# Kernel optimization log

Measured on AMD Instinct MI355X. Metric: run time of the kernel, lower is better.

The kernel has to match this reference:

```python
import jax, jax.numpy as jnp
import numpy as np

NUM_HEADS = 8

def setup_inputs() -> dict:
    key = jax.random.key(0)
    kx, kk, kq, kv, ko = jax.random.split(key, 5)
    B, S, D_in, D_e = 2, 4096, 512, 512
    scale = 1.0 / np.sqrt(D_in)
    x = jax.random.normal(kx, (B, S, D_in), dtype=jnp.float32)
    # nn.Linear(in, out, bias=False) weight has shape (out, in); y = x @ W.T
    W_K = jax.random.normal(kk, (D_e, D_in), dtype=jnp.float32) * scale
    W_Q = jax.random.normal(kq, (D_e, D_in), dtype=jnp.float32) * scale
    W_V = jax.random.normal(kv, (D_e, D_in), dtype=jnp.float32) * scale
    W_O = jax.random.normal(ko, (D_e, D_e), dtype=jnp.float32) * (1.0 / np.sqrt(D_e))
    return {"x": x, "W_K": W_K, "W_Q": W_Q, "W_V": W_V, "W_O": W_O}

def reference(x, W_K, W_Q, W_V, W_O):
    B, S, _ = x.shape
    E = W_K.shape[0]
    H = NUM_HEADS
    d = E // H
    # projections (bias-free linears): y = x @ W.T
    K = jnp.einsum('bsi,ei->bse', x, W_K).reshape(B, S, H, d)
    Q = jnp.einsum('bsi,ei->bse', x, W_Q).reshape(B, S, H, d)
    V = jnp.einsum('bsi,ei->bse', x, W_V).reshape(B, S, H, d)
    # scores with NON-standard scaling: divide by full embed_dim E
    scores = jnp.einsum('bqhd,bkhd->bhqk', Q, K) / E
    weights = jax.nn.softmax(scores, axis=-1)
    wV = jnp.einsum('bhqk,bkhd->bqhd', weights, V).reshape(B, S, E)
    out = jnp.einsum('bse,oe->bso', wV, W_O)
    return out
```

## Files before the change

### kernel.cpp

```cpp
#include <hip/hip_runtime.h>

typedef unsigned short u16;
typedef __attribute__((ext_vector_type(8))) short bf16x8;
typedef __attribute__((ext_vector_type(4))) float f32x4;
typedef __attribute__((ext_vector_type(16))) float f32x16;
typedef __attribute__((ext_vector_type(4))) unsigned int u32x4;

__device__ __forceinline__ u16 f2bf(float f) {
  unsigned u = __builtin_bit_cast(unsigned, f);
  u = u + 0x7fffu + ((u >> 16) & 1u);
  return (u16)(u >> 16);
}

__device__ __forceinline__ float bf2f(u16 u) {
  return __builtin_bit_cast(float, (unsigned)u << 16);
}

__device__ __forceinline__ void gload16(const void* g, void* l) {
  __builtin_amdgcn_global_load_lds((const __attribute__((address_space(1))) unsigned*)g,
                                   (__attribute__((address_space(3))) unsigned*)l, 16, 0, 0);
}

#define MFMA16(a, b, c) __builtin_amdgcn_mfma_f32_16x16x32_bf16(a, b, c, 0, 0, 0)
#define MFMA32(a, b, c) __builtin_amdgcn_mfma_f32_32x32x16_bf16(a, b, c, 0, 0, 0)

__global__ void cvt_kernel(const float* __restrict__ src, u16* __restrict__ dst, int n4, float scale) {
  int i = blockIdx.x * blockDim.x + threadIdx.x;
  if (i >= n4) return;
  const float4 v = ((const float4*)src)[i];
  ushort4 o;
  o.x = f2bf(v.x * scale);
  o.y = f2bf(v.y * scale);
  o.z = f2bf(v.z * scale);
  o.w = f2bf(v.w * scale);
  ((ushort4*)dst)[i] = o;
}

__global__ __launch_bounds__(256) void cvtw_kernel(const float* __restrict__ Wk,
                                                   const float* __restrict__ Wq,
                                                   const float* __restrict__ Wv,
                                                   const float* __restrict__ Wo,
                                                   u16* __restrict__ w1, u16* __restrict__ wo) {
  int i = blockIdx.x * 256 + threadIdx.x;
  int sel = i >> 16, j = i & 65535;
  const float* src = (sel == 0) ? Wk : (sel == 1) ? Wq : (sel == 2) ? Wv : Wo;
  float scale = (sel == 1) ? (1.4426950408889634f / 512.0f) : 1.0f;
  const float4 v = ((const float4*)src)[j];
  ushort4 o;
  o.x = f2bf(v.x * scale);
  o.y = f2bf(v.y * scale);
  o.z = f2bf(v.z * scale);
  o.w = f2bf(v.w * scale);
  if (sel < 3) ((ushort4*)w1)[sel * 65536 + j] = o;
  else         ((ushort4*)wo)[j] = o;
}

template <typename CT>
__global__ __launch_bounds__(256, 2) void gemm_bt(const u16* __restrict__ A,
                                                  const u16* __restrict__ B,
                                                  CT* __restrict__ C, int M, int N, int K,
                                                  u16* __restrict__ VT) {
  __shared__ u16 As[128 * 32];
  __shared__ u16 Bs[128 * 32];
  const int t = threadIdx.x;
  const int lane = t & 63;
  const int w = t >> 6, wr = w >> 1, wc = w & 1;
  const int fr = lane & 15, fq = lane >> 4;
  const long m0 = (long)blockIdx.x * 128, n0 = (long)blockIdx.y * 128;

  f32x4 acc[4][4] = {};

  const int sr = t >> 2;
  const int sc = (t & 3) * 8;
  const u16* Ab = A + (m0 + sr) * (long)K + sc;
  const u16* Bb = B + (n0 + sr) * (long)K + sc;

  for (int k0 = 0; k0 < K; k0 += 32) {
    gload16(Ab + k0, As + t * 8);
    gload16(Ab + 64 * (long)K + k0, As + 2048 + t * 8);
    gload16(Bb + k0, Bs + t * 8);
    gload16(Bb + 64 * (long)K + k0, Bs + 2048 + t * 8);
    __syncthreads();
    bf16x8 a[4], b[4];
#pragma unroll
    for (int i = 0; i < 4; i++)
      a[i] = *(const bf16x8*)(As + (wr * 64 + i * 16 + fr) * 32 + fq * 8);
#pragma unroll
    for (int j = 0; j < 4; j++)
      b[j] = *(const bf16x8*)(Bs + (wc * 64 + j * 16 + fr) * 32 + fq * 8);
#pragma unroll
    for (int i = 0; i < 4; i++)
#pragma unroll
      for (int j = 0; j < 4; j++)
        acc[i][j] = MFMA16(a[i], b[j], acc[i][j]);
    __syncthreads();
  }

  if constexpr (sizeof(CT) == 2) {
    if (VT && n0 >= 1024) {
      const int bb = (int)(m0 >> 12);
      const int s0 = (int)(m0 & 4095) + wr * 64;
      const int hg = (((int)n0 - 1024) >> 6) + wc;
      const long vbase = ((long)(bb * 8 + hg) * 64);
#pragma unroll
      for (int i = 0; i < 4; i++)
#pragma unroll
        for (int j = 0; j < 4; j++) {
          ushort4 o;
          o.x = f2bf(acc[i][j][0]);
          o.y = f2bf(acc[i][j][1]);
          o.z = f2bf(acc[i][j][2]);
          o.w = f2bf(acc[i][j][3]);
          *(ushort4*)(VT + (vbase + j * 16 + fr) * 4096 + s0 + i * 16 + fq * 4) = o;
        }
      return;
    }
  }

#pragma unroll
  for (int i = 0; i < 4; i++)
#pragma unroll
    for (int j = 0; j < 4; j++)
#pragma unroll
      for (int r = 0; r < 4; r++) {
        long m = m0 + wr * 64 + i * 16 + fq * 4 + r;
        long n = n0 + wc * 64 + j * 16 + fr;
        if constexpr (sizeof(CT) == 4)
          C[m * N + n] = acc[i][j][r];
        else
          C[m * N + n] = (CT)f2bf(acc[i][j][r]);
      }
}

template <int NZ>
__global__ __launch_bounds__(512, 4) void attn_kernel(const u16* __restrict__ Y,
                                                      const u16* __restrict__ VT,
                                                      u16* __restrict__ WV,
                                                      u16* __restrict__ PO0,
                                                      u16* __restrict__ PO1,
                                                      float* __restrict__ PD) {
  __shared__ u16 Ks[2][8192];
  __shared__ u16 Vs[2][8192];
  const int t = threadIdx.x;
  const int lane = t & 63, w = t >> 6;
  const int l31 = lane & 31, hi = lane >> 5;
  int orig = blockIdx.x, qb, bh, kh;
  if constexpr (NZ == 2) {
    int logical = (orig & 7) * 64 + (orig >> 3);
    qb = logical & 15; bh = (logical >> 4) & 15; kh = logical >> 8;
  } else {
    int logical = (orig & 7) * 32 + (orig >> 3);
    qb = logical & 15; bh = logical >> 4; kh = 0;
  }
  const int b = bh >> 3, h = bh & 7;
  const long base = (long)b * 4096 * 1536 + h * 64;
  const u16* Kp = Y + base;
  const u16* Qp = Y + base + 512;
  const u16* Vtp = VT + (long)bh * 262144;
  const int q0 = qb * 256 + w * 32;

  int kkv[2], koff[2], vdv[2], voff[2];
#pragma unroll
  for (int r = 0; r < 2; r++) {
    int row = r * 32 + (t >> 4);
    int rx = (t & 15) ^ (row & 15);
    kkv[r] = row * 2 + (rx >> 3);
    koff[r] = (rx & 7) * 8;
    vdv[r] = row;
    voff[r] = rx * 8;
  }

  bf16x8 qf[4];
#pragma unroll
  for (int ks = 0; ks < 4; ks++)
    qf[ks] = *(const bf16x8*)(Qp + (long)(q0 + l31) * 1536 + ks * 16 + hi * 8);

  f32x16 accO[2] = {};
  f32x16 accD = {};
  const u32x4 onesW = {0x3F803F80u, 0x3F803F80u, 0x3F803F80u, 0x3F803F80u};
  const bf16x8 onesB = __builtin_bit_cast(bf16x8, onesW);

  const int kt0 = kh * (32 / NZ), ktN = kt0 + 32 / NZ;

  {
    const int kv0 = kt0 * 128;
#pragma unroll
    for (int r = 0; r < 2; r++) {
      gload16(Kp + (long)(kv0 + kkv[r]) * 1536 + koff[r], &Ks[kt0 & 1][r * 4096 + t * 8]);
      gload16(Vtp + (long)vdv[r] * 4096 + kv0 + voff[r], &Vs[kt0 & 1][r * 4096 + t * 8]);
    }
  }
  __syncthreads();

  for (int kt = kt0; kt < ktN; kt++) {
    const int buf = kt & 1;
    const int kvn = ((kt + 1) & 31) * 128;
#pragma unroll
    for (int r = 0; r < 2; r++) {
      gload16(Kp + (long)(kvn + kkv[r]) * 1536 + koff[r], &Ks[buf ^ 1][r * 4096 + t * 8]);
      gload16(Vtp + (long)vdv[r] * 4096 + kvn + voff[r], &Vs[buf ^ 1][r * 4096 + t * 8]);
    }
    const char* Ksb = (const char*)Ks[buf];
    const char* Vsb = (const char*)Vs[buf];

#pragma unroll
    for (int kv5 = 0; kv5 < 4; kv5++) {
      const int kv = kv5 * 32 + l31;
      const int krow = kv >> 1;
      const int kswz = (krow & 15) << 4;
      const int kpre = ((kv & 1) << 7) | (hi << 4);
      bf16x8 ka[4];
#pragma unroll
      for (int ks = 0; ks < 4; ks++)
        ka[ks] = *(const bf16x8*)(Ksb + krow * 256 + ((kpre | (ks << 5)) ^ kswz));
      f32x16 s0 = {};
#pragma unroll
      for (int ks = 0; ks < 4; ks++)
        s0 = MFMA32(ka[ks], qf[ks], s0);
      unsigned pk0[8];
#pragma unroll
      for (int j = 0; j < 8; j++) {
        float a0 = fmaf(s0[2 * j],     fmaf(s0[2 * j],     0.24022651f, 0.69314718f), 1.0f);
        float a1 = fmaf(s0[2 * j + 1], fmaf(s0[2 * j + 1], 0.24022651f, 0.69314718f), 1.0f);
        pk0[j] = __builtin_amdgcn_perm(__builtin_bit_cast(unsigned, a1),
                                       __builtin_bit_cast(unsigned, a0), 0x07060302u);
      }
#pragma unroll
      for (int s = 0; s < 2; s++) {
        const int bse = s * 4;
        auto rA0 = __builtin_amdgcn_permlane32_swap(pk0[bse + 0], pk0[bse + 2], false, false);
        auto rB0 = __builtin_amdgcn_permlane32_swap(pk0[bse + 1], pk0[bse + 3], false, false);
        u32x4 f0 = {rA0[0], rB0[0], rA0[1], rB0[1]};
        bf16x8 pa0 = __builtin_bit_cast(bf16x8, f0);
        accD = MFMA32(pa0, onesB, accD);
        const int vpre = ((kv5 * 2 + s) << 5) | (hi << 4);
#pragma unroll
        for (int dvb = 0; dvb < 2; dvb++) {
          const int dv = dvb * 32 + l31;
          bf16x8 vb = *(const bf16x8*)(Vsb + dv * 256 + (vpre ^ ((dv & 15) << 4)));
          accO[dvb] = MFMA32(pa0, vb, accO[dvb]);
        }
      }
    }
    __syncthreads();
  }

  const long qgb = (long)b * 4096 + q0;
  if constexpr (NZ == 1) {
#pragma unroll
    for (int r = 0; r < 16; r++) {
      float inv = 1.0f / accD[r];
      long qg = qgb + (r & 3) + 8 * (r >> 2) + 4 * hi;
#pragma unroll
      for (int dvb = 0; dvb < 2; dvb++)
        WV[qg * 512 + h * 64 + dvb * 32 + l31] = f2bf(accO[dvb][r] * inv);
    }
  } else {
    u16* po = kh ? PO1 : PO0;
    float* pd = PD + kh * 65536;
#pragma unroll
    for (int r = 0; r < 16; r++) {
      long qg = qgb + (r & 3) + 8 * (r >> 2) + 4 * hi;
      if (l31 == 0) pd[qg * 8 + h] = accD[r];
#pragma unroll
      for (int dvb = 0; dvb < 2; dvb++)
        po[qg * 512 + h * 64 + dvb * 32 + l31] = f2bf(accO[dvb][r]);
    }
  }
}

__global__ __launch_bounds__(256) void combine_kernel(const u16* __restrict__ PO0,
                                                      const u16* __restrict__ PO1,
                                                      const float* __restrict__ PD,
                                                      u16* __restrict__ WV) {
  int tid = blockIdx.x * 256 + threadIdx.x;
  int q = tid >> 7, e4 = tid & 127;
  int e = e4 * 4, h = e4 >> 4;
  float inv = 1.0f / (PD[q * 8 + h] + PD[65536 + q * 8 + h]);
  ushort4 a = *(const ushort4*)(PO0 + (long)q * 512 + e);
  ushort4 c = *(const ushort4*)(PO1 + (long)q * 512 + e);
  ushort4 o;
  o.x = f2bf((bf2f(a.x) + bf2f(c.x)) * inv);
  o.y = f2bf((bf2f(a.y) + bf2f(c.y)) * inv);
  o.z = f2bf((bf2f(a.z) + bf2f(c.z)) * inv);
  o.w = f2bf((bf2f(a.w) + bf2f(c.w)) * inv);
  *(ushort4*)(WV + (long)q * 512 + e) = o;
}

extern "C" void kernel_launch(void* const* d_in, const int* in_sizes, int n_in,
                              void* d_out, int out_size, void* d_ws, size_t ws_size,
                              hipStream_t stream) {
  (void)in_sizes; (void)n_in; (void)out_size;
  const float* x  = (const float*)d_in[0];
  const float* Wk = (const float*)d_in[1];
  const float* Wq = (const float*)d_in[2];
  const float* Wv = (const float*)d_in[3];
  const float* Wo = (const float*)d_in[4];
  float* out = (float*)d_out;
  char* ws = (char*)d_ws;

  u16* xb = (u16*)ws;
  u16* w1 = (u16*)(ws + 8388608);
  u16* wo = (u16*)(ws + 9961472);
  u16* y  = (u16*)(ws + 10485760);
  u16* wv = (u16*)(ws + 35651584);
  u16* vt = (u16*)(ws + 44040192);
  u16* po1 = (u16*)(ws + 60817408);
  float* pd = (float*)(ws + 69206016);

  cvt_kernel<<<4096, 256, 0, stream>>>(x, xb, 1048576, 1.0f);
  cvtw_kernel<<<1024, 256, 0, stream>>>(Wk, Wq, Wv, Wo, w1, wo);

  gemm_bt<u16><<<dim3(64, 12), 256, 0, stream>>>(xb, w1, y, 8192, 1536, 512, vt);

  if (ws_size >= 69730304ULL) {
    attn_kernel<2><<<512, 512, 0, stream>>>(y, vt, nullptr, xb, po1, pd);
    combine_kernel<<<4096, 256, 0, stream>>>(xb, po1, pd, wv);
  } else {
    attn_kernel<1><<<256, 512, 0, stream>>>(y, vt, wv, nullptr, nullptr, nullptr);
  }
  gemm_bt<float><<<dim3(64, 4), 256, 0, stream>>>(wv, wo, out, 8192, 512, 512, nullptr);
}
```

Before: 124.6 us.

## Fuse split-KV combine into output projection GEMM and merge conversion kernels

Merges the x and weight fp32-to-bf16 conversion kernels into a single launch. It also removes the separate combine kernel: a new output-projection GEMM loads the two partial attention outputs and denominators, normalises them, and writes the bf16 A tile into shared memory before the MFMA loop. This drops two kernel launches and the write-then-read round trip of the combined WV buffer. In exchange, the A operand is loaded synchronously through registers instead of by async global-to-LDS loads, and the GEMM uses smaller 64-row tiles.

Measured after the change: 119.1 us. 4.4% less time.

```diff
diff --git a/kernel.cpp b/kernel.cpp
--- a/kernel.cpp
+++ b/kernel.cpp
@@ -24,35 +24,36 @@
 #define MFMA16(a, b, c) __builtin_amdgcn_mfma_f32_16x16x32_bf16(a, b, c, 0, 0, 0)
 #define MFMA32(a, b, c) __builtin_amdgcn_mfma_f32_32x32x16_bf16(a, b, c, 0, 0, 0)
 
-__global__ void cvt_kernel(const float* __restrict__ src, u16* __restrict__ dst, int n4, float scale) {
-  int i = blockIdx.x * blockDim.x + threadIdx.x;
-  if (i >= n4) return;
-  const float4 v = ((const float4*)src)[i];
-  ushort4 o;
-  o.x = f2bf(v.x * scale);
-  o.y = f2bf(v.y * scale);
-  o.z = f2bf(v.z * scale);
-  o.w = f2bf(v.w * scale);
-  ((ushort4*)dst)[i] = o;
-}
-
-__global__ __launch_bounds__(256) void cvtw_kernel(const float* __restrict__ Wk,
-                                                   const float* __restrict__ Wq,
-                                                   const float* __restrict__ Wv,
-                                                   const float* __restrict__ Wo,
-                                                   u16* __restrict__ w1, u16* __restrict__ wo) {
+__global__ __launch_bounds__(256) void cvt_all(const float* __restrict__ x,
+                                               const float* __restrict__ Wk,
+                                               const float* __restrict__ Wq,
+                                               const float* __restrict__ Wv,
+                                               const float* __restrict__ Wo,
+                                               u16* __restrict__ xb,
+                                               u16* __restrict__ w1,
+                                               u16* __restrict__ wo) {
   int i = blockIdx.x * 256 + threadIdx.x;
-  int sel = i >> 16, j = i & 65535;
-  const float* src = (sel == 0) ? Wk : (sel == 1) ? Wq : (sel == 2) ? Wv : Wo;
-  float scale = (sel == 1) ? (1.4426950408889634f / 512.0f) : 1.0f;
+  const float* src;
+  u16* dst;
+  int j;
+  float scale = 1.0f;
+  if (i < 1048576) {
+    src = x; dst = xb; j = i;
+  } else {
+    int k = i - 1048576;
+    int sel = k >> 16;
+    j = k & 65535;
+    src = (sel == 0) ? Wk : (sel == 1) ? Wq : (sel == 2) ? Wv : Wo;
+    scale = (sel == 1) ? (1.4426950408889634f / 512.0f) : 1.0f;
+    dst = (sel < 3) ? (w1 + (long)sel * 262144) : wo;
+  }
   const float4 v = ((const float4*)src)[j];
   ushort4 o;
   o.x = f2bf(v.x * scale);
   o.y = f2bf(v.y * scale);
   o.z = f2bf(v.z * scale);
   o.w = f2bf(v.w * scale);
-  if (sel < 3) ((ushort4*)w1)[sel * 65536 + j] = o;
-  else         ((ushort4*)wo)[j] = o;
+  ((ushort4*)dst)[j] = o;
 }
 
 template <typename CT>
@@ -129,6 +130,72 @@
           C[m * N + n] = acc[i][j][r];
         else
           C[m * N + n] = (CT)f2bf(acc[i][j][r]);
+      }
+}
+
+__global__ __launch_bounds__(256, 2) void gemm_out(const u16* __restrict__ PO0,
+                                                   const u16* __restrict__ PO1,
+                                                   const float* __restrict__ PD,
+                                                   const u16* __restrict__ B,
+                                                   float* __restrict__ C) {
+  __shared__ u16 As[64 * 32];
+  __shared__ u16 Bs[128 * 32];
+  const int t = threadIdx.x;
+  const int lane = t & 63;
+  const int w = t >> 6, wr = w >> 1, wc = w & 1;
+  const int fr = lane & 15, fq = lane >> 4;
+  const long m0 = (long)blockIdx.x * 64, n0 = (long)blockIdx.y * 128;
+
+  f32x4 acc[2][4] = {};
+
+  const int ar = t >> 2;
+  const int sc = (t & 3) * 8;
+  const long q = m0 + ar;
+  const u16* Ap0 = PO0 + q * 512 + sc;
+  const u16* Ap1 = PO1 + q * 512 + sc;
+  const u16* Bb = B + (n0 + (t >> 2)) * 512L + sc;
+
+  for (int k0 = 0; k0 < 512; k0 += 32) {
+    gload16(Bb + k0, Bs + t * 8);
+    gload16(Bb + 64 * 512 + k0, Bs + 2048 + t * 8);
+    {
+      const int h = (k0 + sc) >> 6;
+      float inv = 1.0f / (PD[q * 8 + h] + PD[65536 + q * 8 + h]);
+      u32x4 o0 = *(const u32x4*)(Ap0 + k0);
+      u32x4 o1 = *(const u32x4*)(Ap1 + k0);
+      u32x4 pk;
+#pragma unroll
+      for (int e = 0; e < 4; e++) {
+        float lo = (bf2f((u16)(o0[e] & 0xffff)) + bf2f((u16)(o1[e] & 0xffff))) * inv;
+        float hi = (bf2f((u16)(o0[e] >> 16)) + bf2f((u16)(o1[e] >> 16))) * inv;
+        pk[e] = (unsigned)f2bf(lo) | ((unsigned)f2bf(hi) << 16);
+      }
+      *(u32x4*)(As + t * 8) = pk;
+    }
+    __syncthreads();
+    bf16x8 a[2], b[4];
+#pragma unroll
+    for (int i = 0; i < 2; i++)
+      a[i] = *(const bf16x8*)(As + (wr * 32 + i * 16 + fr) * 32 + fq * 8);
+#pragma unroll
+    for (int j = 0; j < 4; j++)
+      b[j] = *(const bf16x8*)(Bs + (wc * 64 + j * 16 + fr) * 32 + fq * 8);
+#pragma unroll
+    for (int i = 0; i < 2; i++)
+#pragma unroll
+      for (int j = 0; j < 4; j++)
+        acc[i][j] = MFMA16(a[i], b[j], acc[i][j]);
+    __syncthreads();
+  }
+#pragma unroll
+  for (int i = 0; i < 2; i++)
+#pragma unroll
+    for (int j = 0; j < 4; j++)
+#pragma unroll
+      for (int r = 0; r < 4; r++) {
+        long m = m0 + wr * 32 + i * 16 + fq * 4 + r;
+        long n = n0 + wc * 64 + j * 16 + fr;
+        C[m * 512 + n] = acc[i][j][r];
       }
 }
 
@@ -269,24 +336,6 @@
   }
 }
 
-__global__ __launch_bounds__(256) void combine_kernel(const u16* __restrict__ PO0,
-                                                      const u16* __restrict__ PO1,
-                                                      const float* __restrict__ PD,
-                                                      u16* __restrict__ WV) {
-  int tid = blockIdx.x * 256 + threadIdx.x;
-  int q = tid >> 7, e4 = tid & 127;
-  int e = e4 * 4, h = e4 >> 4;
-  float inv = 1.0f / (PD[q * 8 + h] + PD[65536 + q * 8 + h]);
-  ushort4 a = *(const ushort4*)(PO0 + (long)q * 512 + e);
-  ushort4 c = *(const ushort4*)(PO1 + (long)q * 512 + e);
-  ushort4 o;
-  o.x = f2bf((bf2f(a.x) + bf2f(c.x)) * inv);
-  o.y = f2bf((bf2f(a.y) + bf2f(c.y)) * inv);
-  o.z = f2bf((bf2f(a.z) + bf2f(c.z)) * inv);
-  o.w = f2bf((bf2f(a.w) + bf2f(c.w)) * inv);
-  *(ushort4*)(WV + (long)q * 512 + e) = o;
-}
-
 extern "C" void kernel_launch(void* const* d_in, const int* in_sizes, int n_in,
                               void* d_out, int out_size, void* d_ws, size_t ws_size,
                               hipStream_t stream) {
@@ -308,16 +357,15 @@
   u16* po1 = (u16*)(ws + 60817408);
   float* pd = (float*)(ws + 69206016);
 
-  cvt_kernel<<<4096, 256, 0, stream>>>(x, xb, 1048576, 1.0f);
-  cvtw_kernel<<<1024, 256, 0, stream>>>(Wk, Wq, Wv, Wo, w1, wo);
+  cvt_all<<<5120, 256, 0, stream>>>(x, Wk, Wq, Wv, Wo, xb, w1, wo);
 
   gemm_bt<u16><<<dim3(64, 12), 256, 0, stream>>>(xb, w1, y, 8192, 1536, 512, vt);
 
   if (ws_size >= 69730304ULL) {
     attn_kernel<2><<<512, 512, 0, stream>>>(y, vt, nullptr, xb, po1, pd);
-    combine_kernel<<<4096, 256, 0, stream>>>(xb, po1, pd, wv);
+    gemm_out<<<dim3(128, 4), 256, 0, stream>>>(xb, po1, pd, wo, out);
   } else {
     attn_kernel<1><<<256, 512, 0, stream>>>(y, vt, wv, nullptr, nullptr, nullptr);
-  }
-  gemm_bt<float><<<dim3(64, 4), 256, 0, stream>>>(wv, wo, out, 8192, 512, 512, nullptr);
-}
+    gemm_bt<float><<<dim3(64, 4), 256, 0, stream>>>(wv, wo, out, 8192, 512, 512, nullptr);
+  }
+}
```
